# Performance work log

Measured on AMD Instinct MI355X. Metric: run time of the kernel, lower is better.

The kernel has to match this reference:

```python
import jax, jax.numpy as jnp
import numpy as np

EPS = 1e-5
SLOPE = 0.01  # nn.LeakyReLU default negative_slope


def _bn(x, gamma, beta):
    # BatchNorm1d in training mode: normalize over the voxel (batch) dim
    m = jnp.mean(x, axis=0)
    v = jnp.mean((x - m) ** 2, axis=0)
    return (x - m) * jax.lax.rsqrt(v + EPS) * gamma + beta


def _leaky(x):
    return jnp.where(x >= 0, x, SLOPE * x)


def _sconv(x, W, src, dst, n_out, b=None):
    # spconv gather-GEMM-scatter. src/dst: [K,E] index pairs, one group per
    # 3x3x3 kernel offset. W: [K, Cin, Cout].
    g = jnp.take(x, src, axis=0)                 # [K,E,Cin] gather
    msg = jnp.einsum('kec,kco->keo', g, W)       # [K,E,Cout] per-offset GEMM
    out = jax.ops.segment_sum(msg.reshape(-1, W.shape[-1]),
                              dst.reshape(-1), num_segments=n_out)  # scatter-add
    return out if b is None else out + b


def setup_inputs() -> dict:
    key = jax.random.key(0)
    ks = jax.random.split(key, 16)
    Nf, Nc, K, Ekd, Ekg = 200000, 60000, 27, 40000, 25000
    Cg, Cs, Cn = 128, 64, 64
    s = 0.05
    f32 = jnp.float32
    d = {
        'gate': jax.random.normal(ks[0], (Nc, Cg), f32),
        'shortcut': jax.random.normal(ks[1], (Nf, Cs), f32),
        'src_down': jax.random.randint(ks[2], (K, Ekd), 0, Nf, jnp.int32),
        'dst_down': jax.random.randint(ks[3], (K, Ekd), 0, Nc, jnp.int32),
        'src_g': jax.random.randint(ks[4], (K, Ekg), 0, Nc, jnp.int32),
        'dst_g': jax.random.randint(ks[5], (K, Ekg), 0, Nc, jnp.int32),
        'W_sc': jax.random.normal(ks[6], (K, Cs, Cn), f32) * s,
        'b_sc': jnp.zeros((Cn,), f32),
        'W_g': jax.random.normal(ks[7], (K, Cg, Cn), f32) * s,
        'b_g': jnp.zeros((Cn,), f32),
        'W_gu': jax.random.normal(ks[8], (K, Cn, Cn), f32) * s,
        'b_gu': jnp.zeros((Cn,), f32),
        'W_sum': jax.random.normal(ks[9], (K, Cn, 1), f32) * s,
        'W_up': jax.random.normal(ks[10], (K, 1, Cs), f32) * s,
        'b_up': jnp.zeros((Cs,), f32),
        'gam_sc': jnp.ones((Cn,), f32), 'bet_sc': jnp.zeros((Cn,), f32),
        'gam_g': jnp.ones((Cn,), f32), 'bet_g': jnp.zeros((Cn,), f32),
        'gam_gu': jnp.ones((Cn,), f32), 'bet_gu': jnp.zeros((Cn,), f32),
        'gam_sum': jnp.ones((1,), f32), 'bet_sum': jnp.zeros((1,), f32),
        'gam_up': jnp.ones((Cs,), f32), 'bet_up': jnp.zeros((Cs,), f32),
    }
    return d


def reference(gate, shortcut, src_down, dst_down, src_g, dst_g,
              W_sc, b_sc, W_g, b_g, W_gu, b_gu, W_sum, W_up, b_up,
              gam_sc, bet_sc, gam_g, bet_g, gam_gu, bet_gu,
              gam_sum, bet_sum, gam_up, bet_up):
    Nf, Nc = shortcut.shape[0], gate.shape[0]
    # shortcut branch: stride-2 sparse conv fine -> coarse, BN, LeakyReLU
    theta = _leaky(_bn(_sconv(shortcut, W_sc, src_down, dst_down, Nc, b_sc),
                       gam_sc, bet_sc))
    # gating branch: sparse conv on coarse coords, BN, LeakyReLU
    phi = _leaky(_bn(_sconv(gate, W_g, src_g, dst_g, Nc, b_g), gam_g, bet_g))
    # inverse conv reuses the keyed conv's index pairs transposed (dst<->src)
    phi = _leaky(_bn(_sconv(phi, W_gu, dst_g, src_g, Nc, b_gu), gam_gu, bet_gu))
    # feature-sum fusion + 1-channel submanifold conv
    s = phi + theta
    s = _leaky(_bn(_sconv(s, W_sum, src_g, dst_g, Nc), gam_sum, bet_sum))
    # inverse conv back to fine resolution + sigmoid attention coefficients
    out = jax.nn.sigmoid(_bn(_sconv(s, W_up, dst_down, src_down, Nf, b_up),
                             gam_up, bet_up))
    return out
```

## Files before the change

kernel.cpp:

```cpp
#include <hip/hip_runtime.h>

#define EPS 1e-5f
#define SLOPE 0.01f

__global__ __launch_bounds__(256) void hist_lds(
    const int* __restrict__ scat, int E, int SH, int nb, int* __restrict__ cnt)
{
    __shared__ int h[3136];
    const int k = blockIdx.y;
    const int tid = threadIdx.x;
    for (int i = tid; i < nb; i += 256) h[i] = 0;
    __syncthreads();
    const int* s = scat + (size_t)k * E;
    for (int e = blockIdx.x * 256 + tid; e < E; e += gridDim.x * 256)
        atomicAdd(&h[s[e] >> SH], 1);
    __syncthreads();
    for (int i = tid; i < nb; i += 256) {
        const int v = h[i];
        if (v) atomicAdd(&cnt[i], v);
    }
}

__global__ __launch_bounds__(1024) void scan_kernel(
    const int* __restrict__ cnt, int n, int* __restrict__ offs, int* __restrict__ cur)
{
    __shared__ int part[1024];
    const int tid = threadIdx.x;
    const int chunk = (n + 1023) >> 10;
    const int lo = min(n, tid * chunk), hi = min(n, lo + chunk);
    int s = 0;
    for (int i = lo; i < hi; ++i) s += cnt[i];
    part[tid] = s;
    __syncthreads();
    for (int d = 1; d < 1024; d <<= 1) {
        const int t = (tid >= d) ? part[tid - d] : 0;
        __syncthreads();
        part[tid] += t;
        __syncthreads();
    }
    int run = part[tid] - s;
    for (int i = lo; i < hi; ++i) {
        const int cv = cnt[i];
        offs[i] = run; cur[i] = run; run += cv;
    }
    if (tid == 1023) offs[n] = run;
}

__global__ __launch_bounds__(256) void bucket_kernel(
    const int* __restrict__ gat, const int* __restrict__ scat, int E, int SH,
    int* __restrict__ cur, unsigned* __restrict__ recs)
{
    const int k = blockIdx.y;
    const int* g = gat + (size_t)k * E;
    const int* d = scat + (size_t)k * E;
    for (int e = blockIdx.x * 256 + threadIdx.x; e < E; e += gridDim.x * 256) {
        const int dv = d[e];
        const int key = dv >> SH;
        unsigned rec = (unsigned)g[e] | ((unsigned)(dv & 63) << 16)
                     | ((unsigned)k << 22);
        const int pos = atomicAdd(&cur[key], 1);
        recs[pos] = rec;
    }
}

template<int CHUNKS>
__global__ __launch_bounds__(256) void conv_scatter8(
    const float* __restrict__ x, const float* __restrict__ W,
    const int* __restrict__ src, const int* __restrict__ dst,
    float* __restrict__ acc, int E)
{
    constexpr int CIN = CHUNKS * 64;
    __shared__ float Wl[CIN * 64];
    __shared__ float xl[4][8 * 64];
    const int k   = blockIdx.y;
    const int tid = threadIdx.x;
    const int w   = tid >> 6;
    const int c   = tid & 63;

    const float* Wk = W + (size_t)k * (CIN * 64);
    for (int i = tid * 4; i < CIN * 64; i += 1024)
        *(float4*)&Wl[i] = *(const float4*)&Wk[i];
    __syncthreads();

    const int* srcK = src + (size_t)k * E;
    const int* dstK = dst + (size_t)k * E;
    float* xw = xl[w];
    const int stride = gridDim.x * 32;
    const int last = E - 1;

    int e0 = blockIdx.x * 32 + w * 8;
    if (e0 >= E) return;

    int   q[8];
    float g[8][CHUNKS];
    #pragma unroll
    for (int j = 0; j < 8; ++j) q[j] = srcK[min(e0 + j, last)];
    #pragma unroll
    for (int j = 0; j < 8; ++j)
        #pragma unroll
        for (int h = 0; h < CHUNKS; ++h)
            g[j][h] = x[(size_t)q[j] * CIN + h * 64 + c];

    while (e0 < E) {
        const int ne = E - e0;
        int d[8];
        #pragma unroll
        for (int j = 0; j < 8; ++j) d[j] = dstK[min(e0 + j, last)];
        const int en = e0 + stride;

        float a[8] = {0.f, 0.f, 0.f, 0.f, 0.f, 0.f, 0.f, 0.f};
        #pragma unroll
        for (int h = 0; h < CHUNKS; ++h) {
            #pragma unroll
            for (int j = 0; j < 8; ++j)
                xw[j * 64 + c] = g[j][h];
            if (h == CHUNKS - 1 && en < E) {
                #pragma unroll
                for (int j = 0; j < 8; ++j) q[j] = srcK[min(en + j, last)];
                #pragma unroll
                for (int j = 0; j < 8; ++j)
                    #pragma unroll
                    for (int h2 = 0; h2 < CHUNKS; ++h2)
                        g[j][h2] = x[(size_t)q[j] * CIN + h2 * 64 + c];
            }
            __builtin_amdgcn_wave_barrier();

            #pragma unroll 4
            for (int i = 0; i < 64; i += 4) {
                const float w0 = Wl[(h * 64 + i + 0) * 64 + c];
                const float w1 = Wl[(h * 64 + i + 1) * 64 + c];
                const float w2 = Wl[(h * 64 + i + 2) * 64 + c];
                const float w3 = Wl[(h * 64 + i + 3) * 64 + c];
                #pragma unroll
                for (int j = 0; j < 8; ++j) {
                    const float4 xv = *(const float4*)&xw[j * 64 + i];
                    a[j] = fmaf(xv.w, w3, fmaf(xv.z, w2, fmaf(xv.y, w1, fmaf(xv.x, w0, a[j]))));
                }
            }
            __builtin_amdgcn_wave_barrier();
        }

        #pragma unroll
        for (int j = 0; j < 8; ++j)
            if (j < ne) atomicAdd(&acc[(size_t)d[j] * 64 + c], a[j]);
        e0 = en;
    }
}

__global__ __launch_bounds__(256) void conv_up_gather2(
    const float* __restrict__ s1, const float* __restrict__ Wup,
    const unsigned* __restrict__ recs, const int* __restrict__ offs,
    float* __restrict__ outb, int Nout, float* __restrict__ st)
{
    __shared__ float acc[64 * 64];
    __shared__ float Wl[27 * 64];
    __shared__ float red[512];
    const int p   = blockIdx.x;
    const int tid = threadIdx.x;
    const int w   = tid >> 6;
    const int c   = tid & 63;

    const float4 z = {0.f, 0.f, 0.f, 0.f};
    for (int i = tid * 4; i < 64 * 64; i += 1024) *(float4*)&acc[i] = z;
    for (int i = tid; i < 27 * 64; i += 256) Wl[i] = Wup[i];
    __syncthreads();

    const int lo = offs[p], hi = offs[p + 1];
    int e0 = lo + w * 8;
    if (e0 < hi) {
        const int last = hi - 1;
        unsigned q[8];
        float    v[8];
        #pragma unroll
        for (int j = 0; j < 8; ++j) q[j] = recs[min(e0 + j, last)];
        #pragma unroll
        for (int j = 0; j < 8; ++j) v[j] = s1[q[j] & 0xFFFFu];

        while (e0 < hi) {
            const int ne = hi - e0;
            unsigned d[8];
            float    u[8];
            #pragma unroll
            for (int j = 0; j < 8; ++j) { d[j] = q[j]; u[j] = v[j]; }
            const int en = e0 + 32;
            if (en < hi) {
                const int l2 = hi - 1;
                #pragma unroll
                for (int j = 0; j < 8; ++j) q[j] = recs[min(en + j, l2)];
                #pragma unroll
                for (int j = 0; j < 8; ++j) v[j] = s1[q[j] & 0xFFFFu];
            }
            #pragma unroll
            for (int j = 0; j < 8; ++j)
                if (j < ne)
                    atomicAdd(&acc[(int)((d[j] >> 16) & 63u) * 64 + c],
                              u[j] * Wl[(int)(d[j] >> 22) * 64 + c]);
            e0 = en;
        }
    }
    __syncthreads();

    const int base = p * 64;
    for (int i = tid; i < 64 * 16; i += 256) {
        const int row = base + (i >> 4);
        if (row < Nout)
            *(float4*)&outb[(size_t)row * 64 + (i & 15) * 4] = *(const float4*)&acc[i * 4];
    }

    float s = 0.f, qq = 0.f;
    #pragma unroll
    for (int rr = 0; rr < 16; ++rr) {
        const float vv = acc[(w * 16 + rr) * 64 + c];
        s += vv;
        qq = fmaf(vv, vv, qq);
    }
    red[tid] = s; red[256 + tid] = qq;
    __syncthreads();
    if (tid < 64) {
        atomicAdd(&st[c],      red[c] + red[64 + c] + red[128 + c] + red[192 + c]);
        atomicAdd(&st[64 + c], red[256 + c] + red[320 + c] + red[384 + c] + red[448 + c]);
    }
}

__global__ __launch_bounds__(256) void conv_sum_kernel(
    const float* __restrict__ s, const float* __restrict__ Wsum,
    const int* __restrict__ src, const int* __restrict__ dst,
    float* __restrict__ acc1, int E)
{
    const int k = blockIdx.y;
    __shared__ float Wl[64];
    if (threadIdx.x < 64) Wl[threadIdx.x] = Wsum[k * 64 + threadIdx.x];
    __syncthreads();
    for (int e = blockIdx.x * 256 + threadIdx.x; e < E; e += gridDim.x * 256) {
        const int si = src[(size_t)k * E + e];
        const float4* row = (const float4*)(s + (size_t)si * 64);
        float acc = 0.f;
        #pragma unroll
        for (int q = 0; q < 16; ++q) {
            const float4 v = row[q];
            acc = fmaf(v.x, Wl[q * 4 + 0], acc);
            acc = fmaf(v.y, Wl[q * 4 + 1], acc);
            acc = fmaf(v.z, Wl[q * 4 + 2], acc);
            acc = fmaf(v.w, Wl[q * 4 + 3], acc);
        }
        atomicAdd(&acc1[dst[(size_t)k * E + e]], acc);
    }
}

__global__ __launch_bounds__(256) void stats64(
    const float* __restrict__ x, int N, float* __restrict__ st)
{
    const int c  = threadIdx.x & 63;
    const int rg = threadIdx.x >> 6;
    float s = 0.f, q = 0.f;
    for (int r = blockIdx.x * 4 + rg; r < N; r += gridDim.x * 4) {
        const float v = x[(size_t)r * 64 + c];
        s += v;
        q = fmaf(v, v, q);
    }
    __shared__ float ls[256], lq[256];
    ls[threadIdx.x] = s; lq[threadIdx.x] = q;
    __syncthreads();
    if (threadIdx.x < 64) {
        s = ls[c] + ls[64 + c] + ls[128 + c] + ls[192 + c];
        q = lq[c] + lq[64 + c] + lq[128 + c] + lq[192 + c];
        atomicAdd(&st[c], s);
        atomicAdd(&st[64 + c], q);
    }
}

__global__ __launch_bounds__(256) void stats1(
    const float* __restrict__ x, int N, float* __restrict__ st)
{
    float s = 0.f, q = 0.f;
    for (int i = blockIdx.x * 256 + threadIdx.x; i < N; i += gridDim.x * 256) {
        const float v = x[i];
        s += v;
        q = fmaf(v, v, q);
    }
    __shared__ float ls[256], lq[256];
    ls[threadIdx.x] = s; lq[threadIdx.x] = q;
    __syncthreads();
    for (int off = 128; off > 0; off >>= 1) {
        if (threadIdx.x < off) {
            ls[threadIdx.x] += ls[threadIdx.x + off];
            lq[threadIdx.x] += lq[threadIdx.x + off];
        }
        __syncthreads();
    }
    if (threadIdx.x == 0) { atomicAdd(&st[0], ls[0]); atomicAdd(&st[1], lq[0]); }
}

template<int ACT>
__global__ __launch_bounds__(256) void apply_bn(
    float* __restrict__ x, const float* __restrict__ st, int N, float invN,
    const float* __restrict__ gam, const float* __restrict__ bet,
    const float* __restrict__ add)
{
    __shared__ float sc[64], sh[64];
    if (threadIdx.x < 64) {
        const int c = threadIdx.x;
        const float m = st[c] * invN;
        const float v = st[64 + c] * invN - m * m;
        const float s = rsqrtf(v + EPS) * gam[c];
        sc[c] = s;
        sh[c] = bet[c] - m * s;
    }
    __syncthreads();
    const size_t n = (size_t)N * 64;
    for (size_t i = (size_t)blockIdx.x * 256 + threadIdx.x; i < n;
         i += (size_t)gridDim.x * 256) {
        const int c = (int)(i & 63);
        float y = fmaf(x[i], sc[c], sh[c]);
        if (ACT == 0) y = (y >= 0.f) ? y : SLOPE * y;
        else          y = 1.f / (1.f + __expf(-y));
        if (add) y += add[i];
        x[i] = y;
    }
}

__global__ __launch_bounds__(256) void apply_bn1(
    float* __restrict__ x, const float* __restrict__ st, int N, float invN,
    const float* __restrict__ gam, const float* __restrict__ bet)
{
    const float m  = st[0] * invN;
    const float v  = st[1] * invN - m * m;
    const float s  = rsqrtf(v + EPS) * gam[0];
    const float sh = bet[0] - m * s;
    for (int i = blockIdx.x * 256 + threadIdx.x; i < N; i += gridDim.x * 256) {
        const float y = fmaf(x[i], s, sh);
        x[i] = (y >= 0.f) ? y : SLOPE * y;
    }
}

extern "C" void kernel_launch(void* const* d_in, const int* in_sizes, int n_in,
                              void* d_out, int out_size, void* d_ws, size_t ws_size,
                              hipStream_t stream)
{
    const float* gate     = (const float*)d_in[0];
    const float* shortcut = (const float*)d_in[1];
    const int*   src_down = (const int*)d_in[2];
    const int*   dst_down = (const int*)d_in[3];
    const int*   src_g    = (const int*)d_in[4];
    const int*   dst_g    = (const int*)d_in[5];
    const float* W_sc     = (const float*)d_in[6];
    const float* W_g      = (const float*)d_in[8];
    const float* W_gu     = (const float*)d_in[10];
    const float* W_sum    = (const float*)d_in[12];
    const float* W_up     = (const float*)d_in[13];
    const float* gam_sc   = (const float*)d_in[15];
    const float* bet_sc   = (const float*)d_in[16];
    const float* gam_g    = (const float*)d_in[17];
    const float* bet_g    = (const float*)d_in[18];
    const float* gam_gu   = (const float*)d_in[19];
    const float* bet_gu   = (const float*)d_in[20];
    const float* gam_sum  = (const float*)d_in[21];
    const float* bet_sum  = (const float*)d_in[22];
    const float* gam_up   = (const float*)d_in[23];
    const float* bet_up   = (const float*)d_in[24];

    const int K   = 27;
    const int Nc  = in_sizes[0] / 128;
    const int Nf  = in_sizes[1] / 64;
    const int Ekd = in_sizes[2] / K;
    const int Ekg = in_sizes[4] / K;

    const int SHF = 6;
    const int NBF = (Nf + 63) / 64;

    float* A  = (float*)d_ws;
    float* B  = A + (size_t)Nc * 64;
    float* C  = B + (size_t)Nc * 64;
    float* D  = C + (size_t)Nc * 64;
    float* ST = D + Nc;
    int* cnt4 = (int*)(ST + 640);
    int* off4 = cnt4 + NBF;
    int* cur4 = off4 + NBF + 1;
    unsigned* rec4 = (unsigned*)(cur4 + NBF);

    const size_t zeroBytes = ((size_t)Nc * 64 * 3 + (size_t)Nc + 640) * sizeof(float)
                           + (size_t)NBF * sizeof(int);
    hipMemsetAsync(d_ws, 0, zeroBytes, stream);
    float* out = (float*)d_out;

    const dim3 blk(256);

    hist_lds<<<dim3(4, K), blk, 0, stream>>>(src_down, Ekd, SHF, NBF, cnt4);
    scan_kernel<<<1, 1024, 0, stream>>>(cnt4, NBF, off4, cur4);
    bucket_kernel<<<dim3(64, K), blk, 0, stream>>>(dst_down, src_down, Ekd, SHF, cur4, rec4);

    conv_scatter8<1><<<dim3(56, K), blk, 0, stream>>>(shortcut, W_sc, src_down, dst_down, A, Ekd);
    conv_scatter8<2><<<dim3(75, K), blk, 0, stream>>>(gate, W_g, src_g, dst_g, B, Ekg);

    stats64<<<256, blk, 0, stream>>>(A, Nc, ST + 0);
    stats64<<<256, blk, 0, stream>>>(B, Nc, ST + 128);
    apply_bn<0><<<1024, blk, 0, stream>>>(A, ST + 0,   Nc, 1.0f / Nc, gam_sc, bet_sc, nullptr);
    apply_bn<0><<<1024, blk, 0, stream>>>(B, ST + 128, Nc, 1.0f / Nc, gam_g,  bet_g,  nullptr);

    conv_scatter8<1><<<dim3(56, K), blk, 0, stream>>>(B, W_gu, dst_g, src_g, C, Ekg);
    stats64<<<256, blk, 0, stream>>>(C, Nc, ST + 256);
    apply_bn<0><<<1024, blk, 0, stream>>>(C, ST + 256, Nc, 1.0f / Nc, gam_gu, bet_gu, A);

    conv_sum_kernel<<<dim3(32, K), blk, 0, stream>>>(C, W_sum, src_g, dst_g, D, Ekg);
    stats1<<<256, blk, 0, stream>>>(D, Nc, ST + 384);
    apply_bn1<<<256, blk, 0, stream>>>(D, ST + 384, Nc, 1.0f / Nc, gam_sum, bet_sum);

    conv_up_gather2<<<NBF, blk, 0, stream>>>(D, W_up, rec4, off4, out, Nf, ST + 512);
    apply_bn<1><<<2048, blk, 0, stream>>>(out, ST + 512, Nf, 1.0f / Nf, gam_up, bet_up, nullptr);
}
```

Measured before the change: 1.555 ms.

## Bucket up-conv edges per fine row and fuse paired stats/BN launches

The up-conv's edge bucketing moves from 64-row blocks to individual fine rows, using a full CSR over Nf. Each wave can then accumulate a row in registers with no LDS atomics, and the 16 KB LDS accumulator goes away. The histogram pass now does global atomics per row instead of an LDS histogram, and the single-block scan now covers 200k entries. Separately, the stats and BN-apply launches for the A and B branches are merged into one launch each using a 2-wide grid.

```diff
diff --git a/kernel.cpp b/kernel.cpp
--- a/kernel.cpp
+++ b/kernel.cpp
@@ -3,22 +3,13 @@
 #define EPS 1e-5f
 #define SLOPE 0.01f
 
-__global__ __launch_bounds__(256) void hist_lds(
-    const int* __restrict__ scat, int E, int SH, int nb, int* __restrict__ cnt)
-{
-    __shared__ int h[3136];
+__global__ __launch_bounds__(256) void hist_row(
+    const int* __restrict__ scat, int E, int* __restrict__ cnt)
+{
     const int k = blockIdx.y;
-    const int tid = threadIdx.x;
-    for (int i = tid; i < nb; i += 256) h[i] = 0;
-    __syncthreads();
     const int* s = scat + (size_t)k * E;
-    for (int e = blockIdx.x * 256 + tid; e < E; e += gridDim.x * 256)
-        atomicAdd(&h[s[e] >> SH], 1);
-    __syncthreads();
-    for (int i = tid; i < nb; i += 256) {
-        const int v = h[i];
-        if (v) atomicAdd(&cnt[i], v);
-    }
+    for (int e = blockIdx.x * 256 + threadIdx.x; e < E; e += gridDim.x * 256)
+        atomicAdd(&cnt[s[e]], 1);
 }
 
 __global__ __launch_bounds__(1024) void scan_kernel(
@@ -46,19 +37,16 @@
     if (tid == 1023) offs[n] = run;
 }
 
-__global__ __launch_bounds__(256) void bucket_kernel(
-    const int* __restrict__ gat, const int* __restrict__ scat, int E, int SH,
+__global__ __launch_bounds__(256) void bucket_row(
+    const int* __restrict__ gat, const int* __restrict__ scat, int E,
     int* __restrict__ cur, unsigned* __restrict__ recs)
 {
     const int k = blockIdx.y;
     const int* g = gat + (size_t)k * E;
     const int* d = scat + (size_t)k * E;
     for (int e = blockIdx.x * 256 + threadIdx.x; e < E; e += gridDim.x * 256) {
-        const int dv = d[e];
-        const int key = dv >> SH;
-        unsigned rec = (unsigned)g[e] | ((unsigned)(dv & 63) << 16)
-                     | ((unsigned)k << 22);
-        const int pos = atomicAdd(&cur[key], 1);
+        const unsigned rec = (unsigned)g[e] | ((unsigned)k << 16);
+        const int pos = atomicAdd(&cur[d[e]], 1);
         recs[pos] = rec;
     }
 }
@@ -147,12 +135,11 @@
     }
 }
 
-__global__ __launch_bounds__(256) void conv_up_gather2(
+__global__ __launch_bounds__(256) void conv_up_rows(
     const float* __restrict__ s1, const float* __restrict__ Wup,
     const unsigned* __restrict__ recs, const int* __restrict__ offs,
     float* __restrict__ outb, int Nout, float* __restrict__ st)
 {
-    __shared__ float acc[64 * 64];
     __shared__ float Wl[27 * 64];
     __shared__ float red[512];
     const int p   = blockIdx.x;
@@ -160,61 +147,27 @@
     const int w   = tid >> 6;
     const int c   = tid & 63;
 
-    const float4 z = {0.f, 0.f, 0.f, 0.f};
-    for (int i = tid * 4; i < 64 * 64; i += 1024) *(float4*)&acc[i] = z;
     for (int i = tid; i < 27 * 64; i += 256) Wl[i] = Wup[i];
     __syncthreads();
 
-    const int lo = offs[p], hi = offs[p + 1];
-    int e0 = lo + w * 8;
-    if (e0 < hi) {
-        const int last = hi - 1;
-        unsigned q[8];
-        float    v[8];
-        #pragma unroll
-        for (int j = 0; j < 8; ++j) q[j] = recs[min(e0 + j, last)];
-        #pragma unroll
-        for (int j = 0; j < 8; ++j) v[j] = s1[q[j] & 0xFFFFu];
-
-        while (e0 < hi) {
-            const int ne = hi - e0;
-            unsigned d[8];
-            float    u[8];
-            #pragma unroll
-            for (int j = 0; j < 8; ++j) { d[j] = q[j]; u[j] = v[j]; }
-            const int en = e0 + 32;
-            if (en < hi) {
-                const int l2 = hi - 1;
-                #pragma unroll
-                for (int j = 0; j < 8; ++j) q[j] = recs[min(en + j, l2)];
-                #pragma unroll
-                for (int j = 0; j < 8; ++j) v[j] = s1[q[j] & 0xFFFFu];
-            }
-            #pragma unroll
-            for (int j = 0; j < 8; ++j)
-                if (j < ne)
-                    atomicAdd(&acc[(int)((d[j] >> 16) & 63u) * 64 + c],
-                              u[j] * Wl[(int)(d[j] >> 22) * 64 + c]);
-            e0 = en;
+    float sSum = 0.f, sSq = 0.f;
+    #pragma unroll 1
+    for (int rr = 0; rr < 16; ++rr) {
+        const int r = p * 64 + rr * 4 + w;
+        if (r >= Nout) break;
+        const int lo = offs[r], hi = offs[r + 1];
+        float acc = 0.f;
+        for (int e = lo; e < hi; ++e) {
+            const unsigned rec = recs[e];
+            const float v = s1[rec & 0xFFFFu];
+            acc = fmaf(v, Wl[(int)(rec >> 16) * 64 + c], acc);
         }
-    }
-    __syncthreads();
-
-    const int base = p * 64;
-    for (int i = tid; i < 64 * 16; i += 256) {
-        const int row = base + (i >> 4);
-        if (row < Nout)
-            *(float4*)&outb[(size_t)row * 64 + (i & 15) * 4] = *(const float4*)&acc[i * 4];
-    }
-
-    float s = 0.f, qq = 0.f;
-    #pragma unroll
-    for (int rr = 0; rr < 16; ++rr) {
-        const float vv = acc[(w * 16 + rr) * 64 + c];
-        s += vv;
-        qq = fmaf(vv, vv, qq);
-    }
-    red[tid] = s; red[256 + tid] = qq;
+        outb[(size_t)r * 64 + c] = acc;
+        sSum += acc;
+        sSq = fmaf(acc, acc, sSq);
+    }
+
+    red[tid] = sSum; red[256 + tid] = sSq;
     __syncthreads();
     if (tid < 64) {
         atomicAdd(&st[c],      red[c] + red[64 + c] + red[128 + c] + red[192 + c]);
@@ -247,9 +200,12 @@
     }
 }
 
-__global__ __launch_bounds__(256) void stats64(
-    const float* __restrict__ x, int N, float* __restrict__ st)
-{
+__global__ __launch_bounds__(256) void stats64x2(
+    const float* __restrict__ xa, const float* __restrict__ xb,
+    int N, float* __restrict__ st)
+{
+    const float* x = (blockIdx.y == 0) ? xa : xb;
+    float* sto = st + (size_t)blockIdx.y * 128;
     const int c  = threadIdx.x & 63;
     const int rg = threadIdx.x >> 6;
     float s = 0.f, q = 0.f;
@@ -264,6 +220,28 @@
     if (threadIdx.x < 64) {
         s = ls[c] + ls[64 + c] + ls[128 + c] + ls[192 + c];
         q = lq[c] + lq[64 + c] + lq[128 + c] + lq[192 + c];
+        atomicAdd(&sto[c], s);
+        atomicAdd(&sto[64 + c], q);
+    }
+}
+
+__global__ __launch_bounds__(256) void stats64(
+    const float* __restrict__ x, int N, float* __restrict__ st)
+{
+    const int c  = threadIdx.x & 63;
+    const int rg = threadIdx.x >> 6;
+    float s = 0.f, q = 0.f;
+    for (int r = blockIdx.x * 4 + rg; r < N; r += gridDim.x * 4) {
+        const float v = x[(size_t)r * 64 + c];
+        s += v;
+        q = fmaf(v, v, q);
+    }
+    __shared__ float ls[256], lq[256];
+    ls[threadIdx.x] = s; lq[threadIdx.x] = q;
+    __syncthreads();
+    if (threadIdx.x < 64) {
+        s = ls[c] + ls[64 + c] + ls[128 + c] + ls[192 + c];
+        q = lq[c] + lq[64 + c] + lq[128 + c] + lq[192 + c];
         atomicAdd(&st[c], s);
         atomicAdd(&st[64 + c], q);
     }
@@ -289,6 +267,35 @@
         __syncthreads();
     }
     if (threadIdx.x == 0) { atomicAdd(&st[0], ls[0]); atomicAdd(&st[1], lq[0]); }
+}
+
+__global__ __launch_bounds__(256) void apply_bn2(
+    float* __restrict__ xa, float* __restrict__ xb,
+    const float* __restrict__ st, int N, float invN,
+    const float* __restrict__ gamA, const float* __restrict__ betA,
+    const float* __restrict__ gamB, const float* __restrict__ betB)
+{
+    float* x = (blockIdx.y == 0) ? xa : xb;
+    const float* stp = st + (size_t)blockIdx.y * 128;
+    const float* gam = (blockIdx.y == 0) ? gamA : gamB;
+    const float* bet = (blockIdx.y == 0) ? betA : betB;
+    __shared__ float sc[64], sh[64];
+    if (threadIdx.x < 64) {
+        const int c = threadIdx.x;
+        const float m = stp[c] * invN;
+        const float v = stp[64 + c] * invN - m * m;
+        const float s = rsqrtf(v + EPS) * gam[c];
+        sc[c] = s;
+        sh[c] = bet[c] - m * s;
+    }
+    __syncthreads();
+    const size_t n = (size_t)N * 64;
+    for (size_t i = (size_t)blockIdx.x * 256 + threadIdx.x; i < n;
+         i += (size_t)gridDim.x * 256) {
+        const int c = (int)(i & 63);
+        float y = fmaf(x[i], sc[c], sh[c]);
+        x[i] = (y >= 0.f) ? y : SLOPE * y;
+    }
 }
 
 template<int ACT>
@@ -365,37 +372,33 @@
     const int Ekd = in_sizes[2] / K;
     const int Ekg = in_sizes[4] / K;
 
-    const int SHF = 6;
-    const int NBF = (Nf + 63) / 64;
-
     float* A  = (float*)d_ws;
     float* B  = A + (size_t)Nc * 64;
     float* C  = B + (size_t)Nc * 64;
     float* D  = C + (size_t)Nc * 64;
     float* ST = D + Nc;
-    int* cnt4 = (int*)(ST + 640);
-    int* off4 = cnt4 + NBF;
-    int* cur4 = off4 + NBF + 1;
-    unsigned* rec4 = (unsigned*)(cur4 + NBF);
+    int* cnt5 = (int*)(ST + 640);
+    int* off5 = cnt5 + Nf;
+    int* cur5 = off5 + Nf + 1;
+    unsigned* rec5 = (unsigned*)(cur5 + Nf);
 
     const size_t zeroBytes = ((size_t)Nc * 64 * 3 + (size_t)Nc + 640) * sizeof(float)
-                           + (size_t)NBF * sizeof(int);
+                           + (size_t)Nf * sizeof(int);
     hipMemsetAsync(d_ws, 0, zeroBytes, stream);
     float* out = (float*)d_out;
 
     const dim3 blk(256);
 
-    hist_lds<<<dim3(4, K), blk, 0, stream>>>(src_down, Ekd, SHF, NBF, cnt4);
-    scan_kernel<<<1, 1024, 0, stream>>>(cnt4, NBF, off4, cur4);
-    bucket_kernel<<<dim3(64, K), blk, 0, stream>>>(dst_down, src_down, Ekd, SHF, cur4, rec4);
+    hist_row<<<dim3(32, K), blk, 0, stream>>>(src_down, Ekd, cnt5);
+    scan_kernel<<<1, 1024, 0, stream>>>(cnt5, Nf, off5, cur5);
+    bucket_row<<<dim3(64, K), blk, 0, stream>>>(dst_down, src_down, Ekd, cur5, rec5);
 
     conv_scatter8<1><<<dim3(56, K), blk, 0, stream>>>(shortcut, W_sc, src_down, dst_down, A, Ekd);
     conv_scatter8<2><<<dim3(75, K), blk, 0, stream>>>(gate, W_g, src_g, dst_g, B, Ekg);
 
-    stats64<<<256, blk, 0, stream>>>(A, Nc, ST + 0);
-    stats64<<<256, blk, 0, stream>>>(B, Nc, ST + 128);
-    apply_bn<0><<<1024, blk, 0, stream>>>(A, ST + 0,   Nc, 1.0f / Nc, gam_sc, bet_sc, nullptr);
-    apply_bn<0><<<1024, blk, 0, stream>>>(B, ST + 128, Nc, 1.0f / Nc, gam_g,  bet_g,  nullptr);
+    stats64x2<<<dim3(256, 2), blk, 0, stream>>>(A, B, Nc, ST + 0);
+    apply_bn2<<<dim3(1024, 2), blk, 0, stream>>>(A, B, ST + 0, Nc, 1.0f / Nc,
+                                                 gam_sc, bet_sc, gam_g, bet_g);
 
     conv_scatter8<1><<<dim3(56, K), blk, 0, stream>>>(B, W_gu, dst_g, src_g, C, Ekg);
     stats64<<<256, blk, 0, stream>>>(C, Nc, ST + 256);
@@ -405,6 +408,7 @@
     stats1<<<256, blk, 0, stream>>>(D, Nc, ST + 384);
     apply_bn1<<<256, blk, 0, stream>>>(D, ST + 384, Nc, 1.0f / Nc, gam_sum, bet_sum);
 
-    conv_up_gather2<<<NBF, blk, 0, stream>>>(D, W_up, rec4, off4, out, Nf, ST + 512);
+    const int NBR = (Nf + 63) / 64;
+    conv_up_rows<<<NBR, blk, 0, stream>>>(D, W_up, rec5, off5, out, Nf, ST + 512);
     apply_bn<1><<<2048, blk, 0, stream>>>(out, ST + 512, Nf, 1.0f / Nf, gam_up, bet_up, nullptr);
 }
```

Result: slower. 1.717 ms (+10.4%).
